# Kernel optimization log

Hardware: AMD Instinct MI355X
Metric: run time of the kernel (lower is better)

Reference implementation:

```python
import jax, jax.numpy as jnp
import numpy as np
import math

B, S, D, H = 4, 2048, 1024, 16
DK = D // H

def setup_inputs() -> dict:
    key = jax.random.key(0)
    ks = jax.random.split(key, 12)
    scale = 1.0 / math.sqrt(D)
    inp = {
        "query": jax.random.normal(ks[0], (B, S, D), jnp.float32),
        "key_": jax.random.normal(ks[1], (B, S, D), jnp.float32),
        "value": jax.random.normal(ks[2], (B, S, D), jnp.float32),
        "mask": jnp.broadcast_to(jnp.tril(jnp.ones((S, S), jnp.int32)), (B, S, S)),
        "Wq": jax.random.normal(ks[3], (D, D), jnp.float32) * scale,
        "bq": jnp.zeros((D,), jnp.float32),
        "Wk": jax.random.normal(ks[4], (D, D), jnp.float32) * scale,
        "bk": jnp.zeros((D,), jnp.float32),
        "Wv": jax.random.normal(ks[5], (D, D), jnp.float32) * scale,
        "bv": jnp.zeros((D,), jnp.float32),
        "Wo": jax.random.normal(ks[6], (D, D), jnp.float32) * scale,
        "bo": jnp.zeros((D,), jnp.float32),
    }
    return inp

def reference(query, key_, value, mask, Wq, bq, Wk, bk, Wv, bv, Wo, bo):
    # Linear projections (torch Linear: x @ W^T + b), split into heads [B,H,S,DK]
    def proj(x, W, b):
        y = jnp.einsum('bsd,ed->bse', x, W) + b
        return y.reshape(B, S, H, DK).transpose(0, 2, 1, 3)
    Q = proj(query, Wq, bq)
    K = proj(key_, Wk, bk)
    V = proj(value, Wv, bv)
    # scaled dot-product attention with additive mask-fill
    scores = jnp.einsum('bhqd,bhkd->bhqk', Q, K) / math.sqrt(DK)
    scores = jnp.where(mask[:, None, :, :] == 0, jnp.float32(-1e9), scores)
    attn = jax.nn.softmax(scores, axis=-1)  # dropout p=0.0 (eval) -> identity
    ctx = jnp.einsum('bhqk,bhkd->bhqd', attn, V)
    ctx = ctx.transpose(0, 2, 1, 3).reshape(B, S, D)
    out = jnp.einsum('bsd,ed->bse', ctx, Wo) + bo
    return out
```

## Files before the change

### kernel.cpp

```cpp
#include <hip/hip_runtime.h>
#include <hip/hip_bf16.h>
#include <cstdint>
#include <cstddef>

static constexpr int kB = 4, kS = 2048, kD = 1024, kH = 16, kDK = 64;
static constexpr int kM = kB * kS;

typedef __attribute__((ext_vector_type(8))) __bf16 bf16x8;
typedef __attribute__((ext_vector_type(4))) __bf16 bf16x4;
typedef __attribute__((ext_vector_type(4))) float f32x4;

#define MFMA_BF16(a, b, c) __builtin_amdgcn_mfma_f32_16x16x32_bf16((a), (b), (c), 0, 0, 0)

#define GLDS16(gp, lp)                                                        \
  __builtin_amdgcn_global_load_lds(                                           \
      (__attribute__((address_space(1))) void*)(gp),                          \
      (__attribute__((address_space(3))) void*)(lp), 16, 0, 0)

__device__ __forceinline__ bf16x8 cvt8(const float* s, int i) {
  const float4 a = ((const float4*)s)[i * 2 + 0];
  const float4 b = ((const float4*)s)[i * 2 + 1];
  bf16x8 o;
  o[0] = (__bf16)a.x; o[1] = (__bf16)a.y; o[2] = (__bf16)a.z; o[3] = (__bf16)a.w;
  o[4] = (__bf16)b.x; o[5] = (__bf16)b.y; o[6] = (__bf16)b.z; o[7] = (__bf16)b.w;
  return o;
}

__global__ __launch_bounds__(256) void cvt_f32_bf16(
    const float* __restrict__ src, __bf16* __restrict__ dst, int n8) {
  const int i = blockIdx.x * 256 + threadIdx.x;
  if (i >= n8) return;
  ((bf16x8*)dst)[i] = cvt8(src, i);
}

__global__ __launch_bounds__(256) void cvt_all(
    const float* __restrict__ q, const float* __restrict__ k,
    const float* __restrict__ v, const float* __restrict__ wq,
    const float* __restrict__ wk, const float* __restrict__ wv,
    const float* __restrict__ wo, __bf16* __restrict__ dq,
    __bf16* __restrict__ dk, __bf16* __restrict__ dv,
    __bf16* __restrict__ dwq, __bf16* __restrict__ dwk,
    __bf16* __restrict__ dwv, __bf16* __restrict__ dwo) {
  int bid = blockIdx.x;
  const float* s;
  __bf16* d;
  int i;
  if (bid < 3 * 4096) {
    const int seg = bid >> 12;
    i = (bid & 4095) * 256 + threadIdx.x;
    s = seg == 0 ? q : seg == 1 ? k : v;
    d = seg == 0 ? dq : seg == 1 ? dk : dv;
  } else {
    bid -= 3 * 4096;
    const int seg = bid >> 9;
    i = (bid & 511) * 256 + threadIdx.x;
    s = seg == 0 ? wq : seg == 1 ? wk : seg == 2 ? wv : wo;
    d = seg == 0 ? dwq : seg == 1 ? dwk : seg == 2 ? dwv : dwo;
  }
  ((bf16x8*)d)[i] = cvt8(s, i);
}

template <typename OutT>
__device__ __forceinline__ void gemm_core(
    const __bf16* __restrict__ A, const __bf16* __restrict__ W,
    const float* __restrict__ bias, OutT* __restrict__ out, int mode, int bid,
    __bf16* Sm ) {
  const int tid = threadIdx.x;
  const int wave = tid >> 6, lane = tid & 63;
  const int col = lane & 15, quad = lane >> 4;
  const int m0 = (bid & 63) * 128;
  const int n0 = (bid >> 6) * 128;
  const int wr = (wave & 1) * 64, wc = (wave >> 1) * 64;

  f32x4 acc[4][4] = {};

  const __bf16* srcs[4];
#pragma unroll
  for (int i = 0; i < 4; ++i) {
    const int row = i * 32 + (tid >> 3);
    const int gg = (tid & 7) ^ (row & 7);
    srcs[i] = (gg < 4) ? A + (size_t)(m0 + row) * 1024 + gg * 8
                       : W + (size_t)(n0 + row) * 1024 + (gg - 4) * 8;
  }

  auto stage = [&](int k0, int buf) {
    char* base = (char*)Sm + buf * 16384 + wave * 1024;
#pragma unroll
    for (int i = 0; i < 4; ++i) GLDS16(srcs[i] + k0, base + i * 4096);
  };

  const int ga = ((quad) ^ (col & 7)) * 16;
  const int gw = ((quad + 4) ^ (col & 7)) * 16;

  stage(0, 0);

#pragma unroll 2
  for (int k = 0; k < 32; ++k) {
    __syncthreads();
    if (k < 31) stage((k + 1) * 32, (k + 1) & 1);
    const char* Bp = (const char*)Sm + (k & 1) * 16384;
    bf16x8 af[4], wf[4];
#pragma unroll
    for (int t = 0; t < 4; ++t) {
      af[t] = *(const bf16x8*)(Bp + (wr + t * 16 + col) * 128 + ga);
      wf[t] = *(const bf16x8*)(Bp + (wc + t * 16 + col) * 128 + gw);
    }
#pragma unroll
    for (int rt = 0; rt < 4; ++rt)
#pragma unroll
      for (int ct = 0; ct < 4; ++ct)
        acc[rt][ct] = MFMA_BF16(af[rt], wf[ct], acc[rt][ct]);
  }

#pragma unroll
  for (int ct = 0; ct < 4; ++ct) {
    const int n = n0 + wc + ct * 16 + col;
    const float bb = bias[n];
#pragma unroll
    for (int rt = 0; rt < 4; ++rt) {
#pragma unroll
      for (int r = 0; r < 4; ++r) {
        const int m = m0 + wr + rt * 16 + quad * 4 + r;
        const float v = acc[rt][ct][r] + bb;
        size_t idx;
        if (mode == 0) {
          idx = (size_t)m * 1024 + n;
        } else {
          const int b = m >> 11, s = m & 2047;
          const int h2 = n >> 6, dk = n & 63;
          if (mode == 1)
            idx = ((size_t)(b * 16 + h2) * 2048 + s) * 64 + dk;
          else
            idx = ((size_t)(b * 16 + h2) * 64 + dk) * 2048 + s;
        }
        out[idx] = (OutT)v;
      }
    }
  }
}

template <int MODE, typename OutT>
__global__ __launch_bounds__(256) void gemm_one(
    const __bf16* __restrict__ A, const __bf16* __restrict__ W,
    const float* __restrict__ bias, OutT* __restrict__ out) {
  __shared__ __align__(16) __bf16 Sm[2][128 * 64];
  gemm_core<OutT>(A, W, bias, out, MODE, blockIdx.x, &Sm[0][0]);
}

__global__ __launch_bounds__(256) void gemm_qkv(
    const __bf16* __restrict__ Aq, const __bf16* __restrict__ Ak,
    const __bf16* __restrict__ Av, const __bf16* __restrict__ Wqb,
    const __bf16* __restrict__ Wkb, const __bf16* __restrict__ Wvb,
    const float* __restrict__ bq, const float* __restrict__ bk,
    const float* __restrict__ bv, __bf16* __restrict__ Qw,
    __bf16* __restrict__ Kw, __bf16* __restrict__ Vw) {
  __shared__ __align__(16) __bf16 Sm[2][128 * 64];
  const int seg = blockIdx.x >> 9;
  const int bid = blockIdx.x & 511;
  const __bf16* A = seg == 0 ? Aq : seg == 1 ? Ak : Av;
  const __bf16* W = seg == 0 ? Wqb : seg == 1 ? Wkb : Wvb;
  const float* bias = seg == 0 ? bq : seg == 1 ? bk : bv;
  __bf16* out = seg == 0 ? Qw : seg == 1 ? Kw : Vw;
  gemm_core<__bf16>(A, W, bias, out, seg == 2 ? 2 : 1, bid, &Sm[0][0]);
}

__global__ __launch_bounds__(256, 4) void flash_attn(
    const __bf16* __restrict__ Q, const __bf16* __restrict__ K,
    const __bf16* __restrict__ Vt, __bf16* __restrict__ ctx) {
  __shared__ __align__(16) __bf16 Ks[2][64 * 64];
  __shared__ __align__(16) __bf16 Vs[2][64 * 64];

  const int tid = threadIdx.x;
  const int wave = tid >> 6, lane = tid & 63;
  const int col = lane & 15, quad = lane >> 4;
  const int bh = blockIdx.x >> 4;
  const int pair = blockIdx.x & 15;
  const int b = bh >> 4, h = bh & 15;
  const int t_lo = pair, t_hi = 31 - pair;
  const int q0f[2] = {t_lo * 64 + wave * 16, t_hi * 64 + wave * 16};

  constexpr float SCL = 0.18033688011112042f;

  bf16x8 qf[2][2];
#pragma unroll
  for (int f = 0; f < 2; ++f) {
    const __bf16* Qp = Q + ((size_t)bh * kS + q0f[f] + col) * 64 + quad * 8;
    qf[f][0] = *(const bf16x8*)Qp;
    qf[f][1] = *(const bf16x8*)(Qp + 32);
  }

  f32x4 o[2][4] = {};
  float lsum[2] = {0.f, 0.f};

  const __bf16* Kg = K + (size_t)bh * kS * 64;
  const __bf16* Vg = Vt + (size_t)bh * 64 * kS;

  const int row0 = tid >> 3;
  const int g0 = ((tid & 7) ^ (row0 & 7)) * 8;
  const int ksrc0 = (row0 & ~12) | ((row0 & 4) << 1) | ((row0 & 8) >> 1);

  auto stage = [&](int c, int buf) {
    const int k0 = c * 64;
    char* KB = (char*)Ks[buf] + wave * 1024;
    char* VB = (char*)Vs[buf] + wave * 1024;
    GLDS16(Kg + (size_t)(k0 + ksrc0) * 64 + g0, KB);
    GLDS16(Vg + (size_t)row0 * kS + k0 + g0, VB);
    GLDS16(Kg + (size_t)(k0 + ksrc0 + 32) * 64 + g0, KB + 4096);
    GLDS16(Vg + (size_t)(row0 + 32) * kS + k0 + g0, VB + 4096);
  };

  const int kq0 = ((quad) ^ (col & 7)) * 16;
  const int kq1 = ((quad + 4) ^ (col & 7)) * 16;

  stage(0, 0);

  for (int c = 0; c <= t_hi; ++c) {
    __syncthreads();
    if (c < t_hi) stage(c + 1, (c + 1) & 1);
    const bool lo = (c <= t_lo);
    const bool d0 = (c == t_lo), d1 = (c == t_hi);
    const int k0 = c * 64;
    const char* KB = (const char*)Ks[c & 1];
    const char* VB = (const char*)Vs[c & 1];

    bf16x8 pb[2][2];
#pragma unroll
    for (int kt = 0; kt < 4; ++kt) {
      const int krow = (col & 7) | ((kt & 1) << 3) | ((col & 8) << 1) |
                       ((kt >> 1) << 5);
      const bf16x8 kf0 = *(const bf16x8*)(KB + krow * 128 + kq0);
      const bf16x8 kf1 = *(const bf16x8*)(KB + krow * 128 + kq1);
      f32x4 z = {};
      const f32x4 s1 = MFMA_BF16(kf1, qf[1][1], MFMA_BF16(kf0, qf[1][0], z));
      f32x4 s0 = z;
      if (lo) s0 = MFMA_BF16(kf1, qf[0][1], MFMA_BF16(kf0, qf[0][0], z));
      const int kbase = k0 + (kt >> 1) * 32 + quad * 8 + (kt & 1) * 4;
#pragma unroll
      for (int r = 0; r < 4; ++r) {
        float e1 = __builtin_amdgcn_exp2f(s1[r] * SCL);
        if (d1 && (kbase + r > q0f[1] + col)) e1 = 0.0f;
        lsum[1] += e1;
        pb[1][kt >> 1][(kt & 1) * 4 + r] = (__bf16)e1;
        float e0 = __builtin_amdgcn_exp2f(s0[r] * SCL);
        if (d0 && (kbase + r > q0f[0] + col)) e0 = 0.0f;
        if (lo) lsum[0] += e0;
        pb[0][kt >> 1][(kt & 1) * 4 + r] = (__bf16)e0;
      }
    }
#pragma unroll
    for (int dt = 0; dt < 4; ++dt) {
      const char* vp = VB + (dt * 16 + col) * 128;
      const bf16x8 vf0 = *(const bf16x8*)(vp + kq0);
      const bf16x8 vf1 = *(const bf16x8*)(vp + kq1);
      o[1][dt] = MFMA_BF16(vf1, pb[1][1], MFMA_BF16(vf0, pb[1][0], o[1][dt]));
      if (lo) o[0][dt] = MFMA_BF16(vf1, pb[0][1], MFMA_BF16(vf0, pb[0][0], o[0][dt]));
    }
  }

#pragma unroll
  for (int f = 0; f < 2; ++f) {
    float l = lsum[f];
    l += __shfl_xor(l, 16, 64);
    l += __shfl_xor(l, 32, 64);
    const float inv = 1.0f / l;
    __bf16* cp = ctx + ((size_t)b * kS + q0f[f] + col) * kD + h * 64 + quad * 4;
#pragma unroll
    for (int dt = 0; dt < 4; ++dt) {
      bf16x4 w;
#pragma unroll
      for (int r = 0; r < 4; ++r) w[r] = (__bf16)(o[f][dt][r] * inv);
      *(bf16x4*)(cp + dt * 16) = w;
    }
  }
}

extern "C" void kernel_launch(void* const* d_in, const int* in_sizes, int n_in,
                              void* d_out, int out_size, void* d_ws, size_t ws_size,
                              hipStream_t stream) {
  const float* query = (const float*)d_in[0];
  const float* key_  = (const float*)d_in[1];
  const float* value = (const float*)d_in[2];
  const float* Wq = (const float*)d_in[4];
  const float* bq = (const float*)d_in[5];
  const float* Wk = (const float*)d_in[6];
  const float* bk = (const float*)d_in[7];
  const float* Wv = (const float*)d_in[8];
  const float* bv = (const float*)d_in[9];
  const float* Wo = (const float*)d_in[10];
  const float* bo = (const float*)d_in[11];

  const size_t e = (size_t)kM * kD;
  const size_t w = (size_t)kD * kD;
  float* out = (float*)d_out;

  const size_t REQ = (6 * e + 4 * w) * sizeof(__bf16);

  if (ws_size >= REQ) {
    __bf16* Qw  = (__bf16*)d_ws;
    __bf16* Kw  = Qw + e;
    __bf16* Vw  = Kw + e;
    __bf16* Aq  = Vw + e;
    __bf16* Ak  = Aq + e;
    __bf16* Av  = Ak + e;
    __bf16* Wqb = Av + e;
    __bf16* Wkb = Wqb + w;
    __bf16* Wvb = Wkb + w;
    __bf16* Wob = Wvb + w;

    cvt_all<<<3 * 4096 + 4 * 512, 256, 0, stream>>>(
        query, key_, value, Wq, Wk, Wv, Wo, Aq, Ak, Av, Wqb, Wkb, Wvb, Wob);
    gemm_qkv<<<1536, 256, 0, stream>>>(Aq, Ak, Av, Wqb, Wkb, Wvb, bq, bk, bv,
                                       Qw, Kw, Vw);
    flash_attn<<<kB * kH * 16, 256, 0, stream>>>(Qw, Kw, Vw, Aq);
    gemm_one<0, float><<<512, 256, 0, stream>>>(Aq, Wob, bo, out);
  } else {
    __bf16* Qw = (__bf16*)d_ws;
    __bf16* Kw = Qw + e;
    __bf16* Vw = Kw + e;
    __bf16* Ab = Vw + e;
    __bf16* Wb = Ab + e;

    const int actg = (int)(e / 8 / 256);
    const int wg = (int)(w / 8 / 256);
    cvt_f32_bf16<<<actg, 256, 0, stream>>>(query, Ab, (int)(e / 8));
    cvt_f32_bf16<<<wg, 256, 0, stream>>>(Wq, Wb, (int)(w / 8));
    gemm_one<1, __bf16><<<512, 256, 0, stream>>>(Ab, Wb, bq, Qw);
    cvt_f32_bf16<<<actg, 256, 0, stream>>>(key_, Ab, (int)(e / 8));
    cvt_f32_bf16<<<wg, 256, 0, stream>>>(Wk, Wb, (int)(w / 8));
    gemm_one<1, __bf16><<<512, 256, 0, stream>>>(Ab, Wb, bk, Kw);
    cvt_f32_bf16<<<actg, 256, 0, stream>>>(value, Ab, (int)(e / 8));
    cvt_f32_bf16<<<wg, 256, 0, stream>>>(Wv, Wb, (int)(w / 8));
    gemm_one<2, __bf16><<<512, 256, 0, stream>>>(Ab, Wb, bv, Vw);
    flash_attn<<<kB * kH * 16, 256, 0, stream>>>(Qw, Kw, Vw, Ab);
    cvt_f32_bf16<<<wg, 256, 0, stream>>>(Wo, Wb, (int)(w / 8));
    gemm_one<0, float><<<512, 256, 0, stream>>>(Ab, Wb, bo, out);
  }
}
```

Baseline: 364.4 us.

## Fuse fp32-to-bf16 activation conversion into QKV projection GEMM loads

Removes the separate conversion pass over the query, key and value activations. The QKV GEMM now loads fp32 activations straight into LDS and converts them to bf16 in registers before the MFMA. Only the weights are still pre-converted. This drops one full write and read of the bf16 activation copies, but each GEMM tile now moves twice the activation bytes from global memory and LDS, and adds conversion instructions to the inner loop.

```diff
diff --git a/kernel.cpp b/kernel.cpp
--- a/kernel.cpp
+++ b/kernel.cpp
@@ -33,85 +33,22 @@
   ((bf16x8*)dst)[i] = cvt8(src, i);
 }
 
-__global__ __launch_bounds__(256) void cvt_all(
-    const float* __restrict__ q, const float* __restrict__ k,
-    const float* __restrict__ v, const float* __restrict__ wq,
-    const float* __restrict__ wk, const float* __restrict__ wv,
-    const float* __restrict__ wo, __bf16* __restrict__ dq,
-    __bf16* __restrict__ dk, __bf16* __restrict__ dv,
-    __bf16* __restrict__ dwq, __bf16* __restrict__ dwk,
-    __bf16* __restrict__ dwv, __bf16* __restrict__ dwo) {
-  int bid = blockIdx.x;
-  const float* s;
-  __bf16* d;
-  int i;
-  if (bid < 3 * 4096) {
-    const int seg = bid >> 12;
-    i = (bid & 4095) * 256 + threadIdx.x;
-    s = seg == 0 ? q : seg == 1 ? k : v;
-    d = seg == 0 ? dq : seg == 1 ? dk : dv;
-  } else {
-    bid -= 3 * 4096;
-    const int seg = bid >> 9;
-    i = (bid & 511) * 256 + threadIdx.x;
-    s = seg == 0 ? wq : seg == 1 ? wk : seg == 2 ? wv : wo;
-    d = seg == 0 ? dwq : seg == 1 ? dwk : seg == 2 ? dwv : dwo;
-  }
-  ((bf16x8*)d)[i] = cvt8(s, i);
+__global__ __launch_bounds__(256) void cvt_w4(
+    const float* __restrict__ a, const float* __restrict__ b,
+    const float* __restrict__ c, const float* __restrict__ d,
+    __bf16* __restrict__ da, __bf16* __restrict__ db,
+    __bf16* __restrict__ dc, __bf16* __restrict__ dd) {
+  const int seg = blockIdx.x >> 9;
+  const int i = (blockIdx.x & 511) * 256 + threadIdx.x;
+  const float* s = seg == 0 ? a : seg == 1 ? b : seg == 2 ? c : d;
+  __bf16* o = seg == 0 ? da : seg == 1 ? db : seg == 2 ? dc : dd;
+  ((bf16x8*)o)[i] = cvt8(s, i);
 }
 
 template <typename OutT>
-__device__ __forceinline__ void gemm_core(
-    const __bf16* __restrict__ A, const __bf16* __restrict__ W,
-    const float* __restrict__ bias, OutT* __restrict__ out, int mode, int bid,
-    __bf16* Sm ) {
-  const int tid = threadIdx.x;
-  const int wave = tid >> 6, lane = tid & 63;
-  const int col = lane & 15, quad = lane >> 4;
-  const int m0 = (bid & 63) * 128;
-  const int n0 = (bid >> 6) * 128;
-  const int wr = (wave & 1) * 64, wc = (wave >> 1) * 64;
-
-  f32x4 acc[4][4] = {};
-
-  const __bf16* srcs[4];
-#pragma unroll
-  for (int i = 0; i < 4; ++i) {
-    const int row = i * 32 + (tid >> 3);
-    const int gg = (tid & 7) ^ (row & 7);
-    srcs[i] = (gg < 4) ? A + (size_t)(m0 + row) * 1024 + gg * 8
-                       : W + (size_t)(n0 + row) * 1024 + (gg - 4) * 8;
-  }
-
-  auto stage = [&](int k0, int buf) {
-    char* base = (char*)Sm + buf * 16384 + wave * 1024;
-#pragma unroll
-    for (int i = 0; i < 4; ++i) GLDS16(srcs[i] + k0, base + i * 4096);
-  };
-
-  const int ga = ((quad) ^ (col & 7)) * 16;
-  const int gw = ((quad + 4) ^ (col & 7)) * 16;
-
-  stage(0, 0);
-
-#pragma unroll 2
-  for (int k = 0; k < 32; ++k) {
-    __syncthreads();
-    if (k < 31) stage((k + 1) * 32, (k + 1) & 1);
-    const char* Bp = (const char*)Sm + (k & 1) * 16384;
-    bf16x8 af[4], wf[4];
-#pragma unroll
-    for (int t = 0; t < 4; ++t) {
-      af[t] = *(const bf16x8*)(Bp + (wr + t * 16 + col) * 128 + ga);
-      wf[t] = *(const bf16x8*)(Bp + (wc + t * 16 + col) * 128 + gw);
-    }
-#pragma unroll
-    for (int rt = 0; rt < 4; ++rt)
-#pragma unroll
-      for (int ct = 0; ct < 4; ++ct)
-        acc[rt][ct] = MFMA_BF16(af[rt], wf[ct], acc[rt][ct]);
-  }
-
+__device__ __forceinline__ void gemm_epilogue(
+    f32x4 (&acc)[4][4], const float* __restrict__ bias, OutT* __restrict__ out,
+    int mode, int m0, int n0, int wr, int wc, int col, int quad) {
 #pragma unroll
   for (int ct = 0; ct < 4; ++ct) {
     const int n = n0 + wc + ct * 16 + col;
@@ -139,6 +76,61 @@
   }
 }
 
+template <typename OutT>
+__device__ __forceinline__ void gemm_core(
+    const __bf16* __restrict__ A, const __bf16* __restrict__ W,
+    const float* __restrict__ bias, OutT* __restrict__ out, int mode, int bid,
+    __bf16* Sm ) {
+  const int tid = threadIdx.x;
+  const int wave = tid >> 6, lane = tid & 63;
+  const int col = lane & 15, quad = lane >> 4;
+  const int m0 = (bid & 63) * 128;
+  const int n0 = (bid >> 6) * 128;
+  const int wr = (wave & 1) * 64, wc = (wave >> 1) * 64;
+
+  f32x4 acc[4][4] = {};
+
+  const __bf16* srcs[4];
+#pragma unroll
+  for (int i = 0; i < 4; ++i) {
+    const int row = i * 32 + (tid >> 3);
+    const int gg = (tid & 7) ^ (row & 7);
+    srcs[i] = (gg < 4) ? A + (size_t)(m0 + row) * 1024 + gg * 8
+                       : W + (size_t)(n0 + row) * 1024 + (gg - 4) * 8;
+  }
+
+  auto stage = [&](int k0, int buf) {
+    char* base = (char*)Sm + buf * 16384 + wave * 1024;
+#pragma unroll
+    for (int i = 0; i < 4; ++i) GLDS16(srcs[i] + k0, base + i * 4096);
+  };
+
+  const int ga = ((quad) ^ (col & 7)) * 16;
+  const int gw = ((quad + 4) ^ (col & 7)) * 16;
+
+  stage(0, 0);
+
+#pragma unroll 2
+  for (int k = 0; k < 32; ++k) {
+    __syncthreads();
+    if (k < 31) stage((k + 1) * 32, (k + 1) & 1);
+    const char* Bp = (const char*)Sm + (k & 1) * 16384;
+    bf16x8 af[4], wf[4];
+#pragma unroll
+    for (int t = 0; t < 4; ++t) {
+      af[t] = *(const bf16x8*)(Bp + (wr + t * 16 + col) * 128 + ga);
+      wf[t] = *(const bf16x8*)(Bp + (wc + t * 16 + col) * 128 + gw);
+    }
+#pragma unroll
+    for (int rt = 0; rt < 4; ++rt)
+#pragma unroll
+      for (int ct = 0; ct < 4; ++ct)
+        acc[rt][ct] = MFMA_BF16(af[rt], wf[ct], acc[rt][ct]);
+  }
+
+  gemm_epilogue(acc, bias, out, mode, m0, n0, wr, wc, col, quad);
+}
+
 template <int MODE, typename OutT>
 __global__ __launch_bounds__(256) void gemm_one(
     const __bf16* __restrict__ A, const __bf16* __restrict__ W,
@@ -147,21 +139,107 @@
   gemm_core<OutT>(A, W, bias, out, MODE, blockIdx.x, &Sm[0][0]);
 }
 
-__global__ __launch_bounds__(256) void gemm_qkv(
-    const __bf16* __restrict__ Aq, const __bf16* __restrict__ Ak,
-    const __bf16* __restrict__ Av, const __bf16* __restrict__ Wqb,
+template <typename OutT>
+__device__ __forceinline__ void gemm_core_f32(
+    const float* __restrict__ A, const __bf16* __restrict__ W,
+    const float* __restrict__ bias, OutT* __restrict__ out, int mode, int bid,
+    char* Asm , char* Wsm ) {
+  const int tid = threadIdx.x;
+  const int wave = tid >> 6, lane = tid & 63;
+  const int col = lane & 15, quad = lane >> 4;
+  const int m0 = (bid & 63) * 128;
+  const int n0 = (bid >> 6) * 128;
+  const int wr = (wave & 1) * 64, wc = (wave >> 1) * 64;
+
+  f32x4 acc[4][4] = {};
+
+  const float* asrc[4];
+#pragma unroll
+  for (int i = 0; i < 4; ++i) {
+    const int row = i * 32 + (tid >> 3);
+    const int gg = (tid & 7) ^ (row & 7);
+    asrc[i] = A + (size_t)(m0 + row) * 1024 + gg * 4;
+  }
+  const __bf16* wsrc[2];
+#pragma unroll
+  for (int i = 0; i < 2; ++i) {
+    const int row = i * 64 + (tid >> 2);
+    const int gg = (tid & 3) ^ (row & 3);
+    wsrc[i] = W + (size_t)(n0 + row) * 1024 + gg * 8;
+  }
+
+  auto stage = [&](int k0, int buf) {
+    char* ab = Asm + buf * 16384 + wave * 1024;
+#pragma unroll
+    for (int i = 0; i < 4; ++i) GLDS16(asrc[i] + k0, ab + i * 4096);
+    char* wb = Wsm + buf * 8192 + wave * 1024;
+#pragma unroll
+    for (int i = 0; i < 2; ++i) GLDS16(wsrc[i] + k0, wb + i * 4096);
+  };
+
+  const int c7 = col & 7;
+  const int ga0 = ((2 * quad) ^ c7) * 16;
+  const int ga1 = ((2 * quad + 1) ^ c7) * 16;
+  const int gwf = (quad ^ (col & 3)) * 16;
+
+  stage(0, 0);
+
+#pragma unroll 2
+  for (int k = 0; k < 32; ++k) {
+    __syncthreads();
+    if (k < 31) stage((k + 1) * 32, (k + 1) & 1);
+    const char* Ab = Asm + (k & 1) * 16384;
+    const char* Wb = Wsm + (k & 1) * 8192;
+    bf16x8 af[4], wf[4];
+#pragma unroll
+    for (int t = 0; t < 4; ++t) {
+      const char* ap = Ab + (wr + t * 16 + col) * 128;
+      const f32x4 a0 = *(const f32x4*)(ap + ga0);
+      const f32x4 a1 = *(const f32x4*)(ap + ga1);
+      bf16x8 v;
+#pragma unroll
+      for (int j = 0; j < 4; ++j) {
+        v[j] = (__bf16)a0[j];
+        v[4 + j] = (__bf16)a1[j];
+      }
+      af[t] = v;
+      wf[t] = *(const bf16x8*)(Wb + (wc + t * 16 + col) * 64 + gwf);
+    }
+#pragma unroll
+    for (int rt = 0; rt < 4; ++rt)
+#pragma unroll
+      for (int ct = 0; ct < 4; ++ct)
+        acc[rt][ct] = MFMA_BF16(af[rt], wf[ct], acc[rt][ct]);
+  }
+
+  gemm_epilogue(acc, bias, out, mode, m0, n0, wr, wc, col, quad);
+}
+
+template <int MODE, typename OutT>
+__global__ __launch_bounds__(256) void gemm_one_f32(
+    const float* __restrict__ A, const __bf16* __restrict__ W,
+    const float* __restrict__ bias, OutT* __restrict__ out) {
+  __shared__ __align__(16) char Asm[2 * 16384];
+  __shared__ __align__(16) char Wsm[2 * 8192];
+  gemm_core_f32<OutT>(A, W, bias, out, MODE, blockIdx.x, Asm, Wsm);
+}
+
+__global__ __launch_bounds__(256) void gemm_qkv_f32(
+    const float* __restrict__ Aq, const float* __restrict__ Ak,
+    const float* __restrict__ Av, const __bf16* __restrict__ Wqb,
     const __bf16* __restrict__ Wkb, const __bf16* __restrict__ Wvb,
     const float* __restrict__ bq, const float* __restrict__ bk,
     const float* __restrict__ bv, __bf16* __restrict__ Qw,
     __bf16* __restrict__ Kw, __bf16* __restrict__ Vw) {
-  __shared__ __align__(16) __bf16 Sm[2][128 * 64];
+  __shared__ __align__(16) char Asm[2 * 16384];
+  __shared__ __align__(16) char Wsm[2 * 8192];
   const int seg = blockIdx.x >> 9;
   const int bid = blockIdx.x & 511;
-  const __bf16* A = seg == 0 ? Aq : seg == 1 ? Ak : Av;
+  const float* A = seg == 0 ? Aq : seg == 1 ? Ak : Av;
   const __bf16* W = seg == 0 ? Wqb : seg == 1 ? Wkb : Wvb;
   const float* bias = seg == 0 ? bq : seg == 1 ? bk : bv;
   __bf16* out = seg == 0 ? Qw : seg == 1 ? Kw : Vw;
-  gemm_core<__bf16>(A, W, bias, out, seg == 2 ? 2 : 1, bid, &Sm[0][0]);
+  gemm_core_f32<__bf16>(A, W, bias, out, seg == 2 ? 2 : 1, bid, Asm, Wsm);
 }
 
 __global__ __launch_bounds__(256, 4) void flash_attn(
@@ -293,46 +371,39 @@
   const size_t w = (size_t)kD * kD;
   float* out = (float*)d_out;
 
-  const size_t REQ = (6 * e + 4 * w) * sizeof(__bf16);
+  const size_t REQ = (4 * e + 4 * w) * sizeof(__bf16);
 
   if (ws_size >= REQ) {
     __bf16* Qw  = (__bf16*)d_ws;
     __bf16* Kw  = Qw + e;
     __bf16* Vw  = Kw + e;
-    __bf16* Aq  = Vw + e;
-    __bf16* Ak  = Aq + e;
-    __bf16* Av  = Ak + e;
-    __bf16* Wqb = Av + e;
+    __bf16* Ct  = Vw + e;
+    __bf16* Wqb = Ct + e;
     __bf16* Wkb = Wqb + w;
     __bf16* Wvb = Wkb + w;
     __bf16* Wob = Wvb + w;
 
-    cvt_all<<<3 * 4096 + 4 * 512, 256, 0, stream>>>(
-        query, key_, value, Wq, Wk, Wv, Wo, Aq, Ak, Av, Wqb, Wkb, Wvb, Wob);
-    gemm_qkv<<<1536, 256, 0, stream>>>(Aq, Ak, Av, Wqb, Wkb, Wvb, bq, bk, bv,
-                                       Qw, Kw, Vw);
-    flash_attn<<<kB * kH * 16, 256, 0, stream>>>(Qw, Kw, Vw, Aq);
-    gemm_one<0, float><<<512, 256, 0, stream>>>(Aq, Wob, bo, out);
+    cvt_w4<<<4 * 512, 256, 0, stream>>>(Wq, Wk, Wv, Wo, Wqb, Wkb, Wvb, Wob);
+    gemm_qkv_f32<<<1536, 256, 0, stream>>>(query, key_, value, Wqb, Wkb, Wvb,
+                                           bq, bk, bv, Qw, Kw, Vw);
+    flash_attn<<<kB * kH * 16, 256, 0, stream>>>(Qw, Kw, Vw, Ct);
+    gemm_one<0, float><<<512, 256, 0, stream>>>(Ct, Wob, bo, out);
   } else {
     __bf16* Qw = (__bf16*)d_ws;
     __bf16* Kw = Qw + e;
     __bf16* Vw = Kw + e;
-    __bf16* Ab = Vw + e;
-    __bf16* Wb = Ab + e;
-
-    const int actg = (int)(e / 8 / 256);
+    __bf16* Ct = Vw + e;
+    __bf16* Wb = Ct + e;
+
     const int wg = (int)(w / 8 / 256);
-    cvt_f32_bf16<<<actg, 256, 0, stream>>>(query, Ab, (int)(e / 8));
     cvt_f32_bf16<<<wg, 256, 0, stream>>>(Wq, Wb, (int)(w / 8));
-    gemm_one<1, __bf16><<<512, 256, 0, stream>>>(Ab, Wb, bq, Qw);
-    cvt_f32_bf16<<<actg, 256, 0, stream>>>(key_, Ab, (int)(e / 8));
+    gemm_one_f32<1, __bf16><<<512, 256, 0, stream>>>(query, Wb, bq, Qw);
     cvt_f32_bf16<<<wg, 256, 0, stream>>>(Wk, Wb, (int)(w / 8));
-    gemm_one<1, __bf16><<<512, 256, 0, stream>>>(Ab, Wb, bk, Kw);
-    cvt_f32_bf16<<<actg, 256, 0, stream>>>(value, Ab, (int)(e / 8));
+    gemm_one_f32<1, __bf16><<<512, 256, 0, stream>>>(key_, Wb, bk, Kw);
     cvt_f32_bf16<<<wg, 256, 0, stream>>>(Wv, Wb, (int)(w / 8));
-    gemm_one<2, __bf16><<<512, 256, 0, stream>>>(Ab, Wb, bv, Vw);
-    flash_attn<<<kB * kH * 16, 256, 0, stream>>>(Qw, Kw, Vw, Ab);
+    gemm_one_f32<2, __bf16><<<512, 256, 0, stream>>>(value, Wb, bv, Vw);
+    flash_attn<<<kB * kH * 16, 256, 0, stream>>>(Qw, Kw, Vw, Ct);
     cvt_f32_bf16<<<wg, 256, 0, stream>>>(Wo, Wb, (int)(w / 8));
-    gemm_one<0, float><<<512, 256, 0, stream>>>(Ab, Wb, bo, out);
-  }
-}
+    gemm_one<0, float><<<512, 256, 0, stream>>>(Ct, Wb, bo, out);
+  }
+}
```

Result: slower. 383.9 us (+5.3%).
